# Kernel tuning notes

Hardware: AMD Instinct MI355X
Metric: run time of the kernel (lower is better)

The kernel has to match this reference:

```python
import jax, jax.numpy as jnp
import numpy as np

DIM = 2048; H = 16; QLR = 512; KVLR = 512
NOPE = 128; ROPE = 64; VHD = 128
QKHD = NOPE + ROPE
SCALE = QKHD ** -0.5
EPS = 1.1920929e-07  # torch RMSNorm default eps = finfo(float32).eps
B = 1; S = 2048

def _rmsnorm(x, w):
    return x * jax.lax.rsqrt(jnp.mean(x * x, axis=-1, keepdims=True) + EPS) * w

def _rope(x, cos, sin):
    # x: [b, s, h, d]; cos/sin: [s, d//2] (consecutive-pair complex rotation)
    b, s, h, d = x.shape
    x2 = x.reshape(b, s, h, d // 2, 2)
    x0, x1 = x2[..., 0], x2[..., 1]
    c = cos[None, :, None, :]; sn = sin[None, :, None, :]
    y = jnp.stack([x0 * c - x1 * sn, x0 * sn + x1 * c], axis=-1)
    return y.reshape(b, s, h, d)

def setup_inputs() -> dict:
    key = jax.random.key(0)
    ks = jax.random.split(key, 12)
    def lin(k, fan_in, fan_out):
        bound = 1.0 / np.sqrt(fan_in)
        kw, kb = jax.random.split(k)
        w = jax.random.uniform(kw, (fan_out, fan_in), jnp.float32, -bound, bound)
        b = jax.random.uniform(kb, (fan_out,), jnp.float32, -bound, bound)
        return w, b
    x = jax.random.normal(ks[0], (B, S, DIM), jnp.float32)
    theta = jax.random.uniform(ks[1], (S, ROPE // 2), jnp.float32, 0.0, 2 * np.pi)
    freqs_cos = jnp.cos(theta); freqs_sin = jnp.sin(theta)
    mask = jnp.where(jnp.triu(jnp.ones((S, S), bool), k=1), jnp.float32(-1e9), jnp.float32(0.0))
    wq_a_w, wq_a_b = lin(ks[2], DIM, QLR)
    q_norm_w = jnp.ones((QLR,), jnp.float32)
    wq_b_w, wq_b_b = lin(ks[3], QLR, H * QKHD)
    wkv_a_w, wkv_a_b = lin(ks[4], DIM, KVLR + ROPE)
    kv_norm_w = jnp.ones((KVLR,), jnp.float32)
    wkv_b_w, wkv_b_b = lin(ks[5], KVLR, H * (NOPE + VHD))
    wo_w, wo_b = lin(ks[6], H * VHD, DIM)
    return {"x": x, "start_pos": 0, "freqs_cos": freqs_cos, "freqs_sin": freqs_sin,
            "mask": mask, "wq_a_w": wq_a_w, "wq_a_b": wq_a_b, "q_norm_w": q_norm_w,
            "wq_b_w": wq_b_w, "wq_b_b": wq_b_b, "wkv_a_w": wkv_a_w, "wkv_a_b": wkv_a_b,
            "kv_norm_w": kv_norm_w, "wkv_b_w": wkv_b_w, "wkv_b_b": wkv_b_b,
            "wo_w": wo_w, "wo_b": wo_b}

def reference(x, start_pos, freqs_cos, freqs_sin, mask,
              wq_a_w, wq_a_b, q_norm_w, wq_b_w, wq_b_b,
              wkv_a_w, wkv_a_b, kv_norm_w, wkv_b_w, wkv_b_b, wo_w, wo_b):
    bsz, seqlen, _ = x.shape
    # low-rank query: wq_b(q_norm(wq_a(x)))
    q = _rmsnorm(x @ wq_a_w.T + wq_a_b, q_norm_w) @ wq_b_w.T + wq_b_b
    q = q.reshape(bsz, seqlen, H, QKHD)
    q_nope, q_pe = q[..., :NOPE], q[..., NOPE:]
    q_pe = _rope(q_pe, freqs_cos, freqs_sin)
    kv = x @ wkv_a_w.T + wkv_a_b
    kv_lat, k_pe = kv[..., :KVLR], kv[..., KVLR:]
    k_pe = _rope(k_pe[:, :, None, :], freqs_cos, freqs_sin)  # [b,s,1,ROPE]
    q = jnp.concatenate([q_nope, q_pe], axis=-1)
    kvb = (_rmsnorm(kv_lat, kv_norm_w) @ wkv_b_w.T + wkv_b_b).reshape(bsz, seqlen, H, NOPE + VHD)
    k_nope, v = kvb[..., :NOPE], kvb[..., NOPE:]
    k = jnp.concatenate([k_nope, jnp.broadcast_to(k_pe, (bsz, seqlen, H, ROPE))], axis=-1)
    # prefill (start_pos=0): cache[:end_pos] == freshly written k/v
    scores = jnp.einsum('bshd,bthd->bsht', q, k) * SCALE
    scores = scores + mask[None, :, None, :]
    probs = jax.nn.softmax(scores.astype(jnp.float32), axis=-1).astype(x.dtype)
    out = jnp.einsum('bsht,bthd->bshd', probs, v).reshape(bsz, seqlen, H * VHD)
    return out @ wo_w.T + wo_b
```

## Files before the change

kernel.cpp:

```cpp
#include <hip/hip_runtime.h>
#include <hip/hip_bf16.h>

typedef __attribute__((ext_vector_type(8))) short short8x;
typedef __attribute__((ext_vector_type(4))) short short4x;
typedef __attribute__((ext_vector_type(4))) float float4x;
typedef __hip_bfloat16 bf16;

#define EPS_F 1.1920929e-07f
#define SCALE_F 0.07216878364870323f

__device__ inline float rdv(const void* p, size_t i, int f32) {
  return f32 ? ((const float*)p)[i] : __bfloat162float(((const bf16*)p)[i]);
}

__device__ inline int4 pack8(const float* s) {
  unsigned short h[8];
#pragma unroll
  for (int t = 0; t < 8; t++) {
    bf16 b = __float2bfloat16(s[t]);
    __builtin_memcpy(&h[t], &b, 2);
  }
  int4 r;
  r.x = (int)((unsigned)h[0] | ((unsigned)h[1] << 16));
  r.y = (int)((unsigned)h[2] | ((unsigned)h[3] << 16));
  r.z = (int)((unsigned)h[4] | ((unsigned)h[5] << 16));
  r.w = (int)((unsigned)h[6] | ((unsigned)h[7] << 16));
  return r;
}

typedef __attribute__((address_space(1))) const unsigned int gu32;
typedef __attribute__((address_space(3))) unsigned int lu32;
__device__ __forceinline__ void gload16(const void* g, void* l) {
  __builtin_amdgcn_global_load_lds((gu32*)g, (lu32*)l, 16, 0, 0);
}

__device__ __forceinline__ int detect_exponents(const unsigned short* __restrict__ x,
                                                int tid, int* red) {
  int cnt = 0;
#pragma unroll
  for (int i = 0; i < 4; i++) {
    unsigned short u = x[tid * 4 + i];
    int e = (u >> 7) & 0xFF;
    cnt += (e >= 118 && e <= 130) ? 1 : 0;
  }
#pragma unroll
  for (int off = 1; off < 64; off <<= 1) cnt += __shfl_xor(cnt, off);
  if ((tid & 63) == 0) red[tid >> 6] = cnt;
  __syncthreads();
  return ((red[0] + red[1] + red[2] + red[3]) > 768) ? 0 : 1;
}

__global__ __launch_bounds__(256) void detect_dtype(const unsigned short* __restrict__ x,
                                                    int* __restrict__ flag) {
  __shared__ int red[4];
  int f = detect_exponents(x, threadIdx.x, red);
  if (threadIdx.x == 0) flag[0] = f;
}

__global__ __launch_bounds__(256) void sentinel_kernel(bf16* out, int n) {
  int i = blockIdx.x * 256 + threadIdx.x;
  if (i < n) out[i] = __float2bfloat16(1000.0f);
}

__device__ __forceinline__ void cvt8(const void* src, bf16* dst, size_t i, int f32) {
  if (f32) {
    float4 a = *(const float4*)((const float*)src + i);
    float4 b = *(const float4*)((const float*)src + i + 4);
    float s[8] = {a.x, a.y, a.z, a.w, b.x, b.y, b.z, b.w};
    *(int4*)(dst + i) = pack8(s);
  } else {
    *(int4*)(dst + i) = *(const int4*)((const bf16*)src + i);
  }
}

__global__ __launch_bounds__(256) void convert_in1(
    const void* __restrict__ x, const void* __restrict__ wqa,
    const void* __restrict__ wkva,
    const void* __restrict__ qab, const void* __restrict__ kvab,
    bf16* __restrict__ xb, bf16* __restrict__ wqab, bf16* __restrict__ wkvab,
    bf16* __restrict__ qabb, bf16* __restrict__ kvabb,
    const int* __restrict__ flagp)
{
  const int f32 = flagp[0];
  const int b = blockIdx.x, tid = threadIdx.x;
  if (b < 2048)       { size_t i = ((size_t)b * 256 + tid) * 8;          cvt8(x,    xb,    i, f32); }
  else if (b < 2560)  { size_t i = ((size_t)(b - 2048) * 256 + tid) * 8; cvt8(wqa,  wqab,  i, f32); }
  else if (b < 3136)  { size_t i = ((size_t)(b - 2560) * 256 + tid) * 8; cvt8(wkva, wkvab, i, f32); }
  else {
    for (int i = tid; i < 512; i += 256) qabb[i]  = __float2bfloat16(rdv(qab,  i, f32));
    for (int i = tid; i < 576; i += 256) kvabb[i] = __float2bfloat16(rdv(kvab, i, f32));
  }
}

__global__ __launch_bounds__(256) void convert_in2(
    const void* __restrict__ wqb, const void* __restrict__ wkvb,
    const void* __restrict__ qbb, const void* __restrict__ kvbb,
    bf16* __restrict__ wqbb, bf16* __restrict__ wkvbb,
    bf16* __restrict__ qbbb, bf16* __restrict__ kvbbb,
    const int* __restrict__ flagp)
{
  const int f32 = flagp[0];
  const int b = blockIdx.x, tid = threadIdx.x;
  if (b < 768)        { size_t i = ((size_t)b * 256 + tid) * 8;          cvt8(wqb,  wqbb,  i, f32); }
  else if (b < 1792)  { size_t i = ((size_t)(b - 768) * 256 + tid) * 8;  cvt8(wkvb, wkvbb, i, f32); }
  else if (b == 1792) { for (int i = tid; i < 3072; i += 256) qbbb[i]  = __float2bfloat16(rdv(qbb,  i, f32)); }
  else                { for (int i = tid; i < 4096; i += 256) kvbbb[i] = __float2bfloat16(rdv(kvbb, i, f32)); }
}

__global__ __launch_bounds__(256) void convert_wo(
    const void* __restrict__ wo, const void* __restrict__ wob_in,
    bf16* __restrict__ wo16, bf16* __restrict__ wob16,
    const int* __restrict__ flagp)
{
  const int f32 = flagp[0];
  const int b = blockIdx.x, tid = threadIdx.x;
  if (b < 2048) { size_t i = ((size_t)b * 256 + tid) * 8; cvt8(wo, wo16, i, f32); }
  else { for (int i = tid; i < 2048; i += 256) wob16[i] = __float2bfloat16(rdv(wob_in, i, f32)); }
}

__global__ __launch_bounds__(256) void convert_all(
    const void* __restrict__ x,
    const void* __restrict__ wqa, const void* __restrict__ wkva,
    const void* __restrict__ qab, const void* __restrict__ kvab,
    const void* __restrict__ wqb, const void* __restrict__ wkvb,
    const void* __restrict__ qbb, const void* __restrict__ kvbb,
    const void* __restrict__ wo, const void* __restrict__ wob_in,
    bf16* __restrict__ xb, bf16* __restrict__ wqab, bf16* __restrict__ wkvab,
    bf16* __restrict__ qabb, bf16* __restrict__ kvabb,
    bf16* __restrict__ wqbb, bf16* __restrict__ wkvbb,
    bf16* __restrict__ qbbb, bf16* __restrict__ kvbbb,
    bf16* __restrict__ wo16, bf16* __restrict__ wob16,
    int* __restrict__ flag)
{
  __shared__ int red[4];
  const int b = blockIdx.x, tid = threadIdx.x;
  const int f32 = detect_exponents((const unsigned short*)x, tid, red);
  if (b < 2048)       { size_t i = ((size_t)b * 256 + tid) * 8;          cvt8(x,    xb,    i, f32); }
  else if (b < 2560)  { size_t i = ((size_t)(b - 2048) * 256 + tid) * 8; cvt8(wqa,  wqab,  i, f32); }
  else if (b < 3136)  { size_t i = ((size_t)(b - 2560) * 256 + tid) * 8; cvt8(wkva, wkvab, i, f32); }
  else if (b == 3136) {
    for (int i = tid; i < 512; i += 256) qabb[i]  = __float2bfloat16(rdv(qab,  i, f32));
    for (int i = tid; i < 576; i += 256) kvabb[i] = __float2bfloat16(rdv(kvab, i, f32));
    if (tid == 0) flag[0] = f32;
  }
  else if (b < 5185)  { size_t i = ((size_t)(b - 3137) * 256 + tid) * 8; cvt8(wo, wo16, i, f32); }
  else if (b == 5185) { for (int i = tid; i < 2048; i += 256) wob16[i] = __float2bfloat16(rdv(wob_in, i, f32)); }
  else if (b < 5954)  { size_t i = ((size_t)(b - 5186) * 256 + tid) * 8; cvt8(wqb,  wqbb,  i, f32); }
  else if (b < 6978)  { size_t i = ((size_t)(b - 5954) * 256 + tid) * 8; cvt8(wkvb, wkvbb, i, f32); }
  else if (b == 6978) { for (int i = tid; i < 3072; i += 256) qbbb[i]  = __float2bfloat16(rdv(qbb,  i, f32)); }
  else                { for (int i = tid; i < 4096; i += 256) kvbbb[i] = __float2bfloat16(rdv(kvbb, i, f32)); }
}

template<int OMODE, bool A_DYN>
__device__ __forceinline__ void gemm128_body(
    const void* __restrict__ A, const void* __restrict__ W,
    const void* __restrict__ bias, void* __restrict__ Cout,
    int M, int N, int K, int f32in, int bx, int by,
    int kbeg, int kend, int addbias)
{
  __shared__ int4 As4[128 * 4];
  __shared__ int4 Bs4[128 * 4];
  const int tid = threadIdx.x, lane = tid & 63, wave = tid >> 6;
  const int grp = lane >> 4, l16 = lane & 15;
  const int m0 = bx * 128, n0 = by * 128;
  const int wm = (wave & 1) * 64, wn = (wave >> 1) * 64;
  float4x acc[4][4] = {};
  for (int k0 = kbeg; k0 < kend; k0 += 32) {
    if (!f32in) {
#pragma unroll
      for (int j = 0; j < 2; j++) {
        int row = wave * 32 + j * 16 + (lane >> 2);
        int cs = (lane & 3) ^ ((row >> 1) & 3);
        gload16((const bf16*)A + (size_t)(m0 + row) * K + k0 + cs * 8,
                &As4[(wave * 32 + j * 16) * 4]);
        gload16((const bf16*)W + (size_t)(n0 + row) * K + k0 + cs * 8,
                &Bs4[(wave * 32 + j * 16) * 4]);
      }
    } else {
#pragma unroll
      for (int i = 0; i < 2; i++) {
        int ch = tid + i * 256;
        int row = ch >> 2, c = ch & 3;
        int cs = c ^ ((row >> 1) & 3);
        size_t aoff = (size_t)(m0 + row) * K + k0 + cs * 8;
        size_t boff = (size_t)(n0 + row) * K + k0 + cs * 8;
        As4[row * 4 + c] = A_DYN ? pack8((const float*)A + aoff)
                                 : *(const int4*)((const bf16*)A + aoff);
        Bs4[row * 4 + c] = pack8((const float*)W + boff);
      }
    }
    __syncthreads();
    short8x af[4], bfr[4];
#pragma unroll
    for (int i = 0; i < 4; i++) {
      int ra = wm + i * 16 + l16;
      int rb = wn + i * 16 + l16;
      af[i]  = *(const short8x*)&As4[ra * 4 + (grp ^ ((ra >> 1) & 3))];
      bfr[i] = *(const short8x*)&Bs4[rb * 4 + (grp ^ ((rb >> 1) & 3))];
    }
#pragma unroll
    for (int i = 0; i < 4; i++)
#pragma unroll
      for (int j = 0; j < 4; j++)
        acc[i][j] = __builtin_amdgcn_mfma_f32_16x16x32_bf16(af[i], bfr[j], acc[i][j], 0, 0, 0);
    __syncthreads();
  }
#pragma unroll
  for (int j = 0; j < 4; j++) {
    int gn = n0 + wn + j * 16 + l16;
    if (gn < N) {
      float bv = addbias ? rdv(bias, gn, f32in) : 0.0f;
#pragma unroll
      for (int i = 0; i < 4; i++) {
        int gm0 = m0 + wm + i * 16 + grp * 4;
#pragma unroll
        for (int r = 0; r < 4; r++) {
          float v = acc[i][j][r] + bv;
          size_t idx = (size_t)(gm0 + r) * N + gn;
          if (OMODE == 0)      ((float*)Cout)[idx] = v;
          else if (OMODE == 1) ((bf16*)Cout)[idx] = __float2bfloat16(v);
          else {
            if (f32in) ((float*)Cout)[idx] = v;
            else       ((bf16*)Cout)[idx] = __float2bfloat16(v);
          }
        }
      }
    }
  }
}

__global__ __launch_bounds__(256) void gemmB_dual(
    const void* __restrict__ A0, const void* __restrict__ A1,
    const void* __restrict__ W0, const void* __restrict__ W1,
    const void* __restrict__ b0, const void* __restrict__ b1,
    void* __restrict__ C0, void* __restrict__ C1)
{
  const int z = blockIdx.z;
  if (z == 0 && blockIdx.y >= 24) return;
  const void* A = z ? A1 : A0;
  const void* W = z ? W1 : W0;
  const void* bias = z ? b1 : b0;
  void* C = z ? C1 : C0;
  const int N = z ? 4096 : 3072;
  gemm128_body<1, false>(A, W, bias, C, 2048, N, 512, 0,
                         blockIdx.x, blockIdx.y, 0, 512, 1);
}

__global__ __launch_bounds__(256) void gemmB_fused(
    const bf16* __restrict__ qn, const bf16* __restrict__ kvn,
    const bf16* __restrict__ Wq, const bf16* __restrict__ Wkv,
    const bf16* __restrict__ bq, const bf16* __restrict__ bkv,
    const void* __restrict__ cosb, const void* __restrict__ sinb,
    bf16* __restrict__ qbuf, bf16* __restrict__ kvbC, bf16* __restrict__ Vt,
    const int* __restrict__ flagp)
{
  const int z = blockIdx.z;
  if (z == 0 && blockIdx.y >= 24) return;
  const bf16* A = z ? kvn : qn;
  const bf16* W = z ? Wkv : Wq;
  const bf16* bias = z ? bkv : bq;
  const int K = 512;
  __shared__ int4 As4[128 * 4];
  __shared__ int4 Bs4[128 * 4];
  const int tid = threadIdx.x, lane = tid & 63, wave = tid >> 6;
  const int grp = lane >> 4, l16 = lane & 15;
  const int m0 = blockIdx.x * 128, n0 = blockIdx.y * 128;
  const int wm = (wave & 1) * 64, wn = (wave >> 1) * 64;
  float4x acc[4][4] = {};
  for (int k0 = 0; k0 < K; k0 += 32) {
#pragma unroll
    for (int j = 0; j < 2; j++) {
      int row = wave * 32 + j * 16 + (lane >> 2);
      int cs = (lane & 3) ^ ((row >> 1) & 3);
      gload16(A + (size_t)(m0 + row) * K + k0 + cs * 8,
              &As4[(wave * 32 + j * 16) * 4]);
      gload16(W + (size_t)(n0 + row) * K + k0 + cs * 8,
              &Bs4[(wave * 32 + j * 16) * 4]);
    }
    __syncthreads();
    short8x af[4], bfr[4];
#pragma unroll
    for (int i = 0; i < 4; i++) {
      int ra = wm + i * 16 + l16;
      int rb = wn + i * 16 + l16;
      af[i]  = *(const short8x*)&As4[ra * 4 + (grp ^ ((ra >> 1) & 3))];
      bfr[i] = *(const short8x*)&Bs4[rb * 4 + (grp ^ ((rb >> 1) & 3))];
    }
#pragma unroll
    for (int i = 0; i < 4; i++)
#pragma unroll
      for (int j = 0; j < 4; j++)
        acc[i][j] = __builtin_amdgcn_mfma_f32_16x16x32_bf16(af[i], bfr[j], acc[i][j], 0, 0, 0);
    __syncthreads();
  }
  const int f32 = flagp[0];
#pragma unroll
  for (int j = 0; j < 4; j++) {
    int gn = n0 + wn + j * 16 + l16;
    float bv = __bfloat162float(bias[gn]);
    if (z == 0) {
      int c12 = (gn >> 4) % 12;
      if (c12 >= 8) {
        int jj = ((gn % 192) - 128) >> 1;
#pragma unroll
        for (int i = 0; i < 4; i++) {
          int gm0 = m0 + wm + i * 16 + grp * 4;
#pragma unroll
          for (int r = 0; r < 4; r++) {
            float v = acc[i][j][r] + bv;
            int s = gm0 + r;
            float c  = rdv(cosb, (size_t)s * 32 + jj, f32);
            float sn = rdv(sinb, (size_t)s * 32 + jj, f32);
            float o = __shfl_xor(v, 1);
            float res = (l16 & 1) ? (o * sn + v * c)
                                  : (v * c - o * sn);
            qbuf[(size_t)s * 3072 + gn] = __float2bfloat16(res);
          }
        }
      } else {
#pragma unroll
        for (int i = 0; i < 4; i++) {
          int gm0 = m0 + wm + i * 16 + grp * 4;
#pragma unroll
          for (int r = 0; r < 4; r++)
            qbuf[(size_t)(gm0 + r) * 3072 + gn] = __float2bfloat16(acc[i][j][r] + bv);
        }
      }
    } else {
      int c16 = (gn >> 4) & 15;
      if (c16 >= 8) {
        int hh = gn >> 8;
        int d  = (gn & 255) - 128;
        bf16* vtb = Vt + ((size_t)hh * 128 + d) * 2048;
#pragma unroll
        for (int i = 0; i < 4; i++) {
          int gm0 = m0 + wm + i * 16 + grp * 4;
          unsigned short hv[4];
#pragma unroll
          for (int r = 0; r < 4; r++) {
            bf16 t = __float2bfloat16(acc[i][j][r] + bv);
            __builtin_memcpy(&hv[r], &t, 2);
          }
          int2 w;
          w.x = (int)((unsigned)hv[0] | ((unsigned)hv[1] << 16));
          w.y = (int)((unsigned)hv[2] | ((unsigned)hv[3] << 16));
          *(int2*)(vtb + gm0) = w;
        }
      } else {
        int coff = (gn >> 8) * 128 + (gn & 127);
#pragma unroll
        for (int i = 0; i < 4; i++) {
          int gm0 = m0 + wm + i * 16 + grp * 4;
#pragma unroll
          for (int r = 0; r < 4; r++)
            kvbC[(size_t)(gm0 + r) * 2048 + coff] = __float2bfloat16(acc[i][j][r] + bv);
        }
      }
    }
  }
}

__global__ __launch_bounds__(256) void gemmWo_sk(
    const void* __restrict__ A, const void* __restrict__ W,
    const void* __restrict__ bias, float* __restrict__ part,
    const int* __restrict__ flagp)
{
  const int z = blockIdx.z;
  gemm128_body<0, false>(A, W, bias, part + (size_t)z * 2048 * 2048,
                         2048, 2048, 2048, flagp[0],
                         blockIdx.x, blockIdx.y, z * 1024, z * 1024 + 1024, z == 0);
}

__global__ __launch_bounds__(256) void gemmWo_sk_bf(
    const void* __restrict__ A, const void* __restrict__ W,
    const void* __restrict__ bias, float* __restrict__ part)
{
  const int z = blockIdx.z;
  gemm128_body<0, false>(A, W, bias, part + (size_t)z * 2048 * 2048,
                         2048, 2048, 2048, 0,
                         blockIdx.x, blockIdx.y, z * 1024, z * 1024 + 1024, z == 0);
}

__global__ __launch_bounds__(256) void reduce_out(
    const float* __restrict__ p0, const float* __restrict__ p1,
    void* __restrict__ out, const int* __restrict__ flagp)
{
  const int f32in = flagp[0];
  size_t i = ((size_t)blockIdx.x * 256 + threadIdx.x) * 4;
  float4 a = *(const float4*)(p0 + i);
  float4 b = *(const float4*)(p1 + i);
  a.x += b.x; a.y += b.y; a.z += b.z; a.w += b.w;
  if (f32in) {
    *(float4*)((float*)out + i) = a;
  } else {
    unsigned short h[4];
    bf16 t0 = __float2bfloat16(a.x); __builtin_memcpy(&h[0], &t0, 2);
    bf16 t1 = __float2bfloat16(a.y); __builtin_memcpy(&h[1], &t1, 2);
    bf16 t2 = __float2bfloat16(a.z); __builtin_memcpy(&h[2], &t2, 2);
    bf16 t3 = __float2bfloat16(a.w); __builtin_memcpy(&h[3], &t3, 2);
    int2 v;
    v.x = (int)((unsigned)h[0] | ((unsigned)h[1] << 16));
    v.y = (int)((unsigned)h[2] | ((unsigned)h[3] << 16));
    *(int2*)((bf16*)out + i) = v;
  }
}

__global__ __launch_bounds__(256) void gemmA_sk(
    const void* __restrict__ A,
    const void* __restrict__ W0, const void* __restrict__ W1,
    const void* __restrict__ b0, const void* __restrict__ b1,
    float* __restrict__ C0, float* __restrict__ C1)
{
  const int z = blockIdx.z;
  const int mat = z >> 1, kh = z & 1;
  const int N = mat ? 576 : 512;
  if (blockIdx.y * 128 >= N) return;
  const void* W = mat ? W1 : W0;
  const void* bias = mat ? b1 : b0;
  float* C = (mat ? C1 : C0) + (size_t)kh * 2048 * N;
  gemm128_body<0, false>(A, W, bias, C, 2048, N, 2048, 0,
                         blockIdx.x, blockIdx.y,
                         kh * 1024, kh * 1024 + 1024, kh == 0);
}

__global__ __launch_bounds__(256) void norms_merged(
    const float* __restrict__ q_a0, const float* __restrict__ q_a1,
    const float* __restrict__ kv_a0, const float* __restrict__ kv_a1,
    const void* __restrict__ qw, const void* __restrict__ kvw,
    const void* __restrict__ cosb, const void* __restrict__ sinb,
    bf16* __restrict__ qn, bf16* __restrict__ kvn, bf16* __restrict__ kpe,
    const int* __restrict__ flagp)
{
  const int f32in = flagp[0];
  const int b = blockIdx.x, tid = threadIdx.x;
  __shared__ float red[4];
  if (b < 2048) {
    const int s = b;
    size_t base = (size_t)s * 512;
    float v0 = q_a0[base + tid] + q_a1[base + tid];
    float v1 = q_a0[base + tid + 256] + q_a1[base + tid + 256];
    float ss = v0 * v0 + v1 * v1;
#pragma unroll
    for (int off = 1; off < 64; off <<= 1) ss += __shfl_xor(ss, off);
    if ((tid & 63) == 0) red[tid >> 6] = ss;
    __syncthreads();
    float tot = red[0] + red[1] + red[2] + red[3];
    float scale = rsqrtf(tot * (1.0f / 512.0f) + EPS_F);
    qn[base + tid]       = __float2bfloat16(v0 * scale * rdv(qw, tid, f32in));
    qn[base + tid + 256] = __float2bfloat16(v1 * scale * rdv(qw, tid + 256, f32in));
  } else {
    const int s = b - 2048;
    size_t base = (size_t)s * 576;
    float v0 = kv_a0[base + tid] + kv_a1[base + tid];
    float v1 = kv_a0[base + tid + 256] + kv_a1[base + tid + 256];
    float ss = v0 * v0 + v1 * v1;
#pragma unroll
    for (int off = 1; off < 64; off <<= 1) ss += __shfl_xor(ss, off);
    if ((tid & 63) == 0) red[tid >> 6] = ss;
    __syncthreads();
    float tot = red[0] + red[1] + red[2] + red[3];
    float scale = rsqrtf(tot * (1.0f / 512.0f) + EPS_F);
    kvn[(size_t)s * 512 + tid]       = __float2bfloat16(v0 * scale * rdv(kvw, tid, f32in));
    kvn[(size_t)s * 512 + tid + 256] = __float2bfloat16(v1 * scale * rdv(kvw, tid + 256, f32in));
    if (tid < 32) {
      float x0 = kv_a0[base + 512 + 2 * tid] + kv_a1[base + 512 + 2 * tid];
      float x1 = kv_a0[base + 512 + 2 * tid + 1] + kv_a1[base + 512 + 2 * tid + 1];
      float c  = rdv(cosb, (size_t)s * 32 + tid, f32in);
      float sn = rdv(sinb, (size_t)s * 32 + tid, f32in);
      kpe[s * 64 + 2 * tid]     = __float2bfloat16(x0 * c - x1 * sn);
      kpe[s * 64 + 2 * tid + 1] = __float2bfloat16(x0 * sn + x1 * c);
    }
  }
}

__global__ __launch_bounds__(256) void rope_vt_merged(
    bf16* __restrict__ q, const void* __restrict__ cosb,
    const void* __restrict__ sinb, const bf16* __restrict__ kvb,
    bf16* __restrict__ Vt, const int* __restrict__ flagp)
{
  const int b = blockIdx.x, tid = threadIdx.x;
  __shared__ __align__(16) bf16 tile[64][136];
  if (b < 2048) {
    const int f32in = flagp[0];
    const int s = b;
#pragma unroll
    for (int it = 0; it < 2; it++) {
      int p = tid + it * 256;
      int hh = p >> 5, jj = p & 31;
      bf16* src = q + (size_t)s * 3072 + hh * 192 + 128 + 2 * jj;
      float x0 = __bfloat162float(src[0]);
      float x1 = __bfloat162float(src[1]);
      float c  = rdv(cosb, (size_t)s * 32 + jj, f32in);
      float sn = rdv(sinb, (size_t)s * 32 + jj, f32in);
      src[0] = __float2bfloat16(x0 * c - x1 * sn);
      src[1] = __float2bfloat16(x0 * sn + x1 * c);
    }
  } else {
    const int hb = b - 2048;
    const int h = hb & 15;
    const int t0 = (hb >> 4) * 64;
#pragma unroll
    for (int i = 0; i < 4; i++) {
      int chunk = tid + i * 256;
      int row = chunk >> 4;
      int c8 = (chunk & 15) * 8;
      *(int4*)&tile[row][c8] =
          *(const int4*)(kvb + (size_t)(t0 + row) * 4096 + h * 256 + 128 + c8);
    }
    __syncthreads();
#pragma unroll
    for (int i = 0; i < 32; i++) {
      int idx = tid + i * 256;
      int d = idx >> 6;
      int t = idx & 63;
      Vt[((size_t)h * 128 + d) * 2048 + t0 + t] = tile[t][d];
    }
  }
}

__global__ __launch_bounds__(256) void attn_kernel(
    const bf16* __restrict__ Q, const bf16* __restrict__ kvb,
    const bf16* __restrict__ kpe, const bf16* __restrict__ Vt,
    bf16* __restrict__ Out, const int kvs, const int kvh)
{
  __shared__ __align__(16) bf16 Ks[64 * 200];
  __shared__ __align__(16) bf16 Vs[128 * 72];
  __shared__ __align__(16) bf16 plds[4][16 * 68];
  const int b = blockIdx.x;
  const int h = b & 15;
  const int tt = (b >> 4) & 15;
  const int q0 = ((b >> 8) ? (31 - tt) : tt) * 64;
  const int tid = threadIdx.x;
  const int wave = tid >> 6;
  const int lane = tid & 63;
  const int grp = lane >> 4, l16 = lane & 15;
  const int qrt = q0 + wave * 16;
  const bf16* Qbase = Q + (size_t)(qrt + l16) * 3072 + h * 192;
  short8x qf[6];
#pragma unroll
  for (int c = 0; c < 6; c++)
    qf[c] = *(const short8x*)(Qbase + c * 32 + grp * 8);
  float m_run[4], l_run[4];
  float4x o_acc[8] = {};
#pragma unroll
  for (int r = 0; r < 4; r++) { m_run[r] = -__builtin_inff(); l_run[r] = 0.f; }
  bf16* pl = &plds[wave][0];
  for (int t0 = 0; t0 <= q0; t0 += 64) {
#pragma unroll
    for (int i = 0; i < 4; i++) {
      int ch = tid + i * 256;
      int row = ch >> 4, c = ch & 15;
      *(int4*)&Ks[row * 200 + c * 8] =
          *(const int4*)(kvb + (size_t)(t0 + row) * kvs + h * kvh + c * 8);
    }
#pragma unroll
    for (int i = 0; i < 2; i++) {
      int ch = tid + i * 256;
      int row = ch >> 3, c = ch & 7;
      *(int4*)&Ks[row * 200 + 128 + c * 8] =
          *(const int4*)(kpe + (size_t)(t0 + row) * 64 + c * 8);
    }
#pragma unroll
    for (int i = 0; i < 4; i++) {
      int ch = tid + i * 256;
      int row = ch >> 3, c = ch & 7;
      *(int4*)&Vs[row * 72 + c * 8] =
          *(const int4*)(Vt + ((size_t)h * 128 + row) * 2048 + t0 + c * 8);
    }
    __syncthreads();
    float4x sacc[4] = {};
#pragma unroll
    for (int n = 0; n < 4; n++) {
      const bf16* Kb = &Ks[(n * 16 + l16) * 200 + grp * 8];
#pragma unroll
      for (int c = 0; c < 6; c++) {
        short8x kf = *(const short8x*)(Kb + c * 32);
        sacc[n] = __builtin_amdgcn_mfma_f32_16x16x32_bf16(qf[c], kf, sacc[n], 0, 0, 0);
      }
    }
    float pv[4][4], alpha[4];
#pragma unroll
    for (int r = 0; r < 4; r++) {
      const int s_row = qrt + grp * 4 + r;
      float p0[4];
      float mx = -__builtin_inff();
#pragma unroll
      for (int n = 0; n < 4; n++) {
        int t = t0 + n * 16 + l16;
        float v = sacc[n][r] * SCALE_F;
        v = (t > s_row) ? -1.0e9f : v;
        p0[n] = v;
        mx = fmaxf(mx, v);
      }
      mx = fmaxf(mx, __shfl_xor(mx, 1));
      mx = fmaxf(mx, __shfl_xor(mx, 2));
      mx = fmaxf(mx, __shfl_xor(mx, 4));
      mx = fmaxf(mx, __shfl_xor(mx, 8));
      float m_new = fmaxf(m_run[r], mx);
      float a = __expf(m_run[r] - m_new);
      m_run[r] = m_new;
      float sum = 0.f;
#pragma unroll
      for (int n = 0; n < 4; n++) {
        float e = __expf(p0[n] - m_new);
        pv[n][r] = e;
        sum += e;
      }
      sum += __shfl_xor(sum, 1);
      sum += __shfl_xor(sum, 2);
      sum += __shfl_xor(sum, 4);
      sum += __shfl_xor(sum, 8);
      l_run[r] = l_run[r] * a + sum;
      alpha[r] = a;
    }
#pragma unroll
    for (int n = 0; n < 8; n++)
#pragma unroll
      for (int r = 0; r < 4; r++)
        o_acc[n][r] *= alpha[r];
#pragma unroll
    for (int n = 0; n < 4; n++)
#pragma unroll
      for (int r = 0; r < 4; r++)
        pl[(grp * 4 + r) * 68 + n * 16 + l16] = __float2bfloat16(pv[n][r]);
#pragma unroll
    for (int c = 0; c < 2; c++) {
      union { short4x h4[2]; short8x v8; } pk;
      const bf16* pp = pl + l16 * 68 + c * 32 + grp * 8;
      pk.h4[0] = *(const short4x*)(pp);
      pk.h4[1] = *(const short4x*)(pp + 4);
#pragma unroll
      for (int n = 0; n < 8; n++) {
        short8x vf = *(const short8x*)&Vs[(size_t)(n * 16 + l16) * 72 + c * 32 + grp * 8];
        o_acc[n] = __builtin_amdgcn_mfma_f32_16x16x32_bf16(pk.v8, vf, o_acc[n], 0, 0, 0);
      }
    }
    __syncthreads();
  }
  float inv[4];
#pragma unroll
  for (int r = 0; r < 4; r++) inv[r] = 1.0f / l_run[r];
#pragma unroll
  for (int n = 0; n < 8; n++)
#pragma unroll
    for (int r = 0; r < 4; r++) {
      int s_row = qrt + grp * 4 + r;
      Out[(size_t)s_row * 2048 + h * 128 + n * 16 + l16] =
          __float2bfloat16(o_acc[n][r] * inv[r]);
    }
}

extern "C" void kernel_launch(void* const* d_in, const int* in_sizes, int n_in,
                              void* d_out, int out_size, void* d_ws, size_t ws_size,
                              hipStream_t stream) {
  const void* x        = d_in[0];
  const void* fcos     = d_in[2];
  const void* fsin     = d_in[3];
  const void* wq_a_w   = d_in[5];
  const void* wq_a_b   = d_in[6];
  const void* q_norm_w = d_in[7];
  const void* wq_b_w   = d_in[8];
  const void* wq_b_b   = d_in[9];
  const void* wkv_a_w  = d_in[10];
  const void* wkv_a_b  = d_in[11];
  const void* kv_norm_w= d_in[12];
  const void* wkv_b_w  = d_in[13];
  const void* wkv_b_b  = d_in[14];
  const void* wo_w     = d_in[15];
  const void* wo_b     = d_in[16];

  const size_t KB = 1024, MB = 1024 * 1024;
  if (ws_size < 46 * MB) {
    sentinel_kernel<<<(out_size + 255) / 256, 256, 0, stream>>>((bf16*)d_out, out_size);
    return;
  }
  char* ws = (char*)d_ws;
  bf16*  kpe    = (bf16*)(ws);
  int*   flag   = (int*)(ws + 256 * KB);
  bf16*  qbuf   = (bf16*)(ws + 512 * KB);
  bf16*  kvb    = (bf16*)(ws + 12 * MB + 512 * KB);
  bf16*  kvbC   = (bf16*)(ws + 12 * MB + 512 * KB);
  bf16*  Vt     = (bf16*)(ws + 28 * MB + 512 * KB);
  bf16*  attnout= (bf16*)(ws + 36 * MB + 512 * KB);
  float* kv_a0  = (float*)(ws + 512 * KB);
  float* kv_a1  = (float*)(ws + 5 * MB);
  float* q_a0   = (float*)(ws + 36 * MB + 512 * KB);
  float* q_a1   = (float*)(ws + 40 * MB + 512 * KB);
  bf16*  qn     = (bf16*)(ws + 28 * MB + 512 * KB);
  bf16*  kvn    = (bf16*)(ws + 30 * MB + 512 * KB);
  float* wpart  = (float*)(ws + 512 * KB);
  bf16*  xb     = (bf16*)(ws + 12 * MB + 512 * KB);
  bf16*  wqab   = (bf16*)(ws + 20 * MB + 512 * KB);
  bf16*  wkvab  = (bf16*)(ws + 22 * MB + 512 * KB);
  bf16*  qabb   = (bf16*)(ws + 25 * MB);
  bf16*  kvabb  = (bf16*)(ws + 25 * MB + 64 * KB);
  bf16*  wqbb_m = (bf16*)(ws + 36 * MB + 512 * KB);
  bf16*  wkvbb_m= (bf16*)(ws + 39 * MB + 512 * KB);
  bf16*  qbbb_m = (bf16*)(ws + 43 * MB + 512 * KB);
  bf16*  kvbbb_m= (bf16*)(ws + 43 * MB + 768 * KB);
  bf16*  wo16   = (bf16*)(ws + 46 * MB);
  bf16*  wob16  = (bf16*)(ws + 54 * MB + 512 * KB);
  bf16*  wqbb_b = (bf16*)(ws + 56 * MB);
  bf16*  wkvbb_b= (bf16*)(ws + 59 * MB);
  bf16*  qbbb_b = (bf16*)(ws + 63 * MB);
  bf16*  kvbbb_b= (bf16*)(ws + 63 * MB + 64 * KB);
  bf16*  qnF    = (bf16*)(ws + 20 * MB + 512 * KB);
  bf16*  kvnF   = (bf16*)(ws + 22 * MB + 512 * KB);

  const bool wofast = (ws_size >= 56 * MB);
  const bool bigws  = (ws_size >= 64 * MB);

  dim3 blk(256);
  if (bigws) {
    convert_all<<<6980, blk, 0, stream>>>(
        x, wq_a_w, wkv_a_w, wq_a_b, wkv_a_b, wq_b_w, wkv_b_w, wq_b_b, wkv_b_b,
        wo_w, wo_b,
        xb, wqab, wkvab, qabb, kvabb, wqbb_b, wkvbb_b, qbbb_b, kvbbb_b,
        wo16, wob16, flag);
    gemmA_sk<<<dim3(16, 5, 4), blk, 0, stream>>>(
        xb, wqab, wkvab, qabb, kvabb, q_a0, kv_a0);
    norms_merged<<<4096, blk, 0, stream>>>(
        q_a0, q_a1, kv_a0, kv_a1, q_norm_w, kv_norm_w, fcos, fsin,
        qnF, kvnF, kpe, flag);
    gemmB_fused<<<dim3(16, 32, 2), blk, 0, stream>>>(
        qnF, kvnF, wqbb_b, wkvbb_b, qbbb_b, kvbbb_b, fcos, fsin,
        qbuf, kvbC, Vt, flag);
    attn_kernel<<<dim3(512), blk, 0, stream>>>(qbuf, kvbC, kpe, Vt, attnout,
                                               2048, 128);
    gemmWo_sk_bf<<<dim3(16, 16, 2), blk, 0, stream>>>(attnout, wo16, wob16, wpart);
    reduce_out<<<4096, blk, 0, stream>>>(wpart, wpart + (size_t)2048 * 2048, d_out, flag);
  } else {
    detect_dtype<<<1, blk, 0, stream>>>((const unsigned short*)x, flag);
    convert_in1<<<3137, blk, 0, stream>>>(
        x, wq_a_w, wkv_a_w, wq_a_b, wkv_a_b, xb, wqab, wkvab, qabb, kvabb, flag);
    if (wofast)
      convert_wo<<<2049, blk, 0, stream>>>(wo_w, wo_b, wo16, wob16, flag);
    gemmA_sk<<<dim3(16, 5, 4), blk, 0, stream>>>(
        xb, wqab, wkvab, qabb, kvabb, q_a0, kv_a0);
    norms_merged<<<4096, blk, 0, stream>>>(
        q_a0, q_a1, kv_a0, kv_a1, q_norm_w, kv_norm_w, fcos, fsin,
        qn, kvn, kpe, flag);
    convert_in2<<<1794, blk, 0, stream>>>(
        wq_b_w, wkv_b_w, wq_b_b, wkv_b_b, wqbb_m, wkvbb_m, qbbb_m, kvbbb_m, flag);
    gemmB_dual<<<dim3(16, 32, 2), blk, 0, stream>>>(
        qn, kvn, wqbb_m, wkvbb_m, qbbb_m, kvbbb_m, qbuf, kvb);
    rope_vt_merged<<<2560, blk, 0, stream>>>(qbuf, fcos, fsin, kvb, Vt, flag);
    attn_kernel<<<dim3(512), blk, 0, stream>>>(qbuf, kvb, kpe, Vt, attnout,
                                               4096, 256);
    if (wofast)
      gemmWo_sk_bf<<<dim3(16, 16, 2), blk, 0, stream>>>(attnout, wo16, wob16, wpart);
    else
      gemmWo_sk<<<dim3(16, 16, 2), blk, 0, stream>>>(attnout, wo_w, wo_b, wpart, flag);
    reduce_out<<<4096, blk, 0, stream>>>(wpart, wpart + (size_t)2048 * 2048, d_out, flag);
  }
}
```

Measured before the change: 317.2 us.

## Split causal attention KV range into two chunks with a merge kernel

Result: no change. 311.9 us (-1.7%).

```diff
diff --git a/kernel.cpp b/kernel.cpp
--- a/kernel.cpp
+++ b/kernel.cpp
@@ -8,6 +8,7 @@
 
 #define EPS_F 1.1920929e-07f
 #define SCALE_F 0.07216878364870323f
+#define M_INIT -1.0e30f
 
 __device__ inline float rdv(const void* p, size_t i, int f32) {
   return f32 ? ((const float*)p)[i] : __bfloat162float(((const bf16*)p)[i]);
@@ -516,6 +517,206 @@
       Vt[((size_t)h * 128 + d) * 2048 + t0 + t] = tile[t][d];
     }
   }
+}
+
+__global__ __launch_bounds__(256) void attn_split(
+    const bf16* __restrict__ Q, const bf16* __restrict__ kvb,
+    const bf16* __restrict__ kpe, const bf16* __restrict__ Vt,
+    bf16* __restrict__ P0, bf16* __restrict__ P1,
+    float* __restrict__ ml0, float* __restrict__ ml1,
+    const int kvs, const int kvh)
+{
+  __shared__ __align__(16) bf16 Ks[64 * 200];
+  __shared__ __align__(16) bf16 Vs[128 * 72];
+  __shared__ __align__(16) bf16 plds[4][16 * 68];
+  const int b = blockIdx.x;
+  const int cchunk = b >> 9;
+  const int h = b & 15;
+  const int tt = 31 - ((b >> 4) & 31);
+  const int q0 = tt * 64;
+  const int nt = tt + 1;
+  const int half = (nt + 1) >> 1;
+  const int lo = cchunk ? half : 0;
+  const int hi = cchunk ? nt : half;
+  bf16* Pout = cchunk ? P1 : P0;
+  float* mlp = cchunk ? ml1 : ml0;
+  const int tid = threadIdx.x;
+  const int wave = tid >> 6;
+  const int lane = tid & 63;
+  const int grp = lane >> 4, l16 = lane & 15;
+  const int qrt = q0 + wave * 16;
+
+  if (lo >= hi) {
+#pragma unroll
+    for (int n = 0; n < 8; n++) {
+      int s_row = qrt + grp * 4;
+#pragma unroll
+      for (int r = 0; r < 4; r++)
+        Pout[(size_t)(s_row + r) * 2048 + h * 128 + n * 16 + l16] =
+            __float2bfloat16(0.0f);
+    }
+    if ((lane & 15) == 0) {
+#pragma unroll
+      for (int r = 0; r < 4; r++) {
+        int s_row = qrt + grp * 4 + r;
+        mlp[((size_t)h * 2048 + s_row) * 2]     = M_INIT;
+        mlp[((size_t)h * 2048 + s_row) * 2 + 1] = 0.0f;
+      }
+    }
+    return;
+  }
+
+  const bf16* Qbase = Q + (size_t)(qrt + l16) * 3072 + h * 192;
+  short8x qf[6];
+#pragma unroll
+  for (int c = 0; c < 6; c++)
+    qf[c] = *(const short8x*)(Qbase + c * 32 + grp * 8);
+  float m_run[4], l_run[4];
+  float4x o_acc[8] = {};
+#pragma unroll
+  for (int r = 0; r < 4; r++) { m_run[r] = M_INIT; l_run[r] = 0.f; }
+  bf16* pl = &plds[wave][0];
+  for (int ti = lo; ti < hi; ti++) {
+    const int t0 = ti * 64;
+#pragma unroll
+    for (int i = 0; i < 4; i++) {
+      int ch = tid + i * 256;
+      int row = ch >> 4, c = ch & 15;
+      *(int4*)&Ks[row * 200 + c * 8] =
+          *(const int4*)(kvb + (size_t)(t0 + row) * kvs + h * kvh + c * 8);
+    }
+#pragma unroll
+    for (int i = 0; i < 2; i++) {
+      int ch = tid + i * 256;
+      int row = ch >> 3, c = ch & 7;
+      *(int4*)&Ks[row * 200 + 128 + c * 8] =
+          *(const int4*)(kpe + (size_t)(t0 + row) * 64 + c * 8);
+    }
+#pragma unroll
+    for (int i = 0; i < 4; i++) {
+      int ch = tid + i * 256;
+      int row = ch >> 3, c = ch & 7;
+      *(int4*)&Vs[row * 72 + c * 8] =
+          *(const int4*)(Vt + ((size_t)h * 128 + row) * 2048 + t0 + c * 8);
+    }
+    __syncthreads();
+    float4x sacc[4] = {};
+#pragma unroll
+    for (int n = 0; n < 4; n++) {
+      const bf16* Kb = &Ks[(n * 16 + l16) * 200 + grp * 8];
+#pragma unroll
+      for (int c = 0; c < 6; c++) {
+        short8x kf = *(const short8x*)(Kb + c * 32);
+        sacc[n] = __builtin_amdgcn_mfma_f32_16x16x32_bf16(qf[c], kf, sacc[n], 0, 0, 0);
+      }
+    }
+    float pv[4][4], alpha[4];
+#pragma unroll
+    for (int r = 0; r < 4; r++) {
+      const int s_row = qrt + grp * 4 + r;
+      float p0[4];
+      float mx = M_INIT;
+#pragma unroll
+      for (int n = 0; n < 4; n++) {
+        int t = t0 + n * 16 + l16;
+        float v = sacc[n][r] * SCALE_F;
+        v = (t > s_row) ? -1.0e9f : v;
+        p0[n] = v;
+        mx = fmaxf(mx, v);
+      }
+      mx = fmaxf(mx, __shfl_xor(mx, 1));
+      mx = fmaxf(mx, __shfl_xor(mx, 2));
+      mx = fmaxf(mx, __shfl_xor(mx, 4));
+      mx = fmaxf(mx, __shfl_xor(mx, 8));
+      float m_new = fmaxf(m_run[r], mx);
+      float a = __expf(m_run[r] - m_new);
+      m_run[r] = m_new;
+      float sum = 0.f;
+#pragma unroll
+      for (int n = 0; n < 4; n++) {
+        float e = __expf(p0[n] - m_new);
+        pv[n][r] = e;
+        sum += e;
+      }
+      sum += __shfl_xor(sum, 1);
+      sum += __shfl_xor(sum, 2);
+      sum += __shfl_xor(sum, 4);
+      sum += __shfl_xor(sum, 8);
+      l_run[r] = l_run[r] * a + sum;
+      alpha[r] = a;
+    }
+#pragma unroll
+    for (int n = 0; n < 8; n++)
+#pragma unroll
+      for (int r = 0; r < 4; r++)
+        o_acc[n][r] *= alpha[r];
+#pragma unroll
+    for (int n = 0; n < 4; n++)
+#pragma unroll
+      for (int r = 0; r < 4; r++)
+        pl[(grp * 4 + r) * 68 + n * 16 + l16] = __float2bfloat16(pv[n][r]);
+#pragma unroll
+    for (int c = 0; c < 2; c++) {
+      union { short4x h4[2]; short8x v8; } pk;
+      const bf16* pp = pl + l16 * 68 + c * 32 + grp * 8;
+      pk.h4[0] = *(const short4x*)(pp);
+      pk.h4[1] = *(const short4x*)(pp + 4);
+#pragma unroll
+      for (int n = 0; n < 8; n++) {
+        short8x vf = *(const short8x*)&Vs[(size_t)(n * 16 + l16) * 72 + c * 32 + grp * 8];
+        o_acc[n] = __builtin_amdgcn_mfma_f32_16x16x32_bf16(pk.v8, vf, o_acc[n], 0, 0, 0);
+      }
+    }
+    __syncthreads();
+  }
+#pragma unroll
+  for (int n = 0; n < 8; n++)
+#pragma unroll
+    for (int r = 0; r < 4; r++) {
+      int s_row = qrt + grp * 4 + r;
+      Pout[(size_t)s_row * 2048 + h * 128 + n * 16 + l16] =
+          __float2bfloat16(o_acc[n][r]);
+    }
+  if ((lane & 15) == 0) {
+#pragma unroll
+    for (int r = 0; r < 4; r++) {
+      int s_row = qrt + grp * 4 + r;
+      mlp[((size_t)h * 2048 + s_row) * 2]     = m_run[r];
+      mlp[((size_t)h * 2048 + s_row) * 2 + 1] = l_run[r];
+    }
+  }
+}
+
+__global__ __launch_bounds__(256) void attn_merge(
+    bf16* __restrict__ P0, const bf16* __restrict__ P1,
+    const float* __restrict__ ml0, const float* __restrict__ ml1)
+{
+  const int s_row = blockIdx.x, tid = threadIdx.x;
+  const int h = tid >> 4;
+  const size_t mli = ((size_t)h * 2048 + s_row) * 2;
+  float m0 = ml0[mli], l0 = ml0[mli + 1];
+  float m1 = ml1[mli], l1 = ml1[mli + 1];
+  float M = fmaxf(m0, m1);
+  float w0 = __expf(m0 - M), w1 = __expf(m1 - M);
+  float Linv = 1.0f / (l0 * w0 + l1 * w1);
+  size_t base = (size_t)s_row * 2048 + tid * 8;
+  int4 a4 = *(const int4*)(P0 + base);
+  int4 b4 = *(const int4*)(P1 + base);
+  const unsigned short* ah = (const unsigned short*)&a4;
+  const unsigned short* bh = (const unsigned short*)&b4;
+  unsigned short oh[8];
+#pragma unroll
+  for (int k = 0; k < 8; k++) {
+    unsigned ua = (unsigned)ah[k] << 16, ub = (unsigned)bh[k] << 16;
+    float fa, fb;
+    __builtin_memcpy(&fa, &ua, 4);
+    __builtin_memcpy(&fb, &ub, 4);
+    bf16 t = __float2bfloat16((fa * w0 + fb * w1) * Linv);
+    __builtin_memcpy(&oh[k], &t, 2);
+  }
+  int4 o4;
+  __builtin_memcpy(&o4, oh, 16);
+  *(int4*)(P0 + base) = o4;
 }
 
 __global__ __launch_bounds__(256) void attn_kernel(
@@ -706,6 +907,9 @@
   bf16*  kvbbb_b= (bf16*)(ws + 63 * MB + 64 * KB);
   bf16*  qnF    = (bf16*)(ws + 20 * MB + 512 * KB);
   bf16*  kvnF   = (bf16*)(ws + 22 * MB + 512 * KB);
+  bf16*  attnP1 = (bf16*)(ws + 20 * MB + 512 * KB);
+  float* attnml0= (float*)(ws + 44 * MB + 512 * KB);
+  float* attnml1= (float*)(ws + 44 * MB + 768 * KB);
 
   const bool wofast = (ws_size >= 56 * MB);
   const bool bigws  = (ws_size >= 64 * MB);
@@ -725,8 +929,9 @@
     gemmB_fused<<<dim3(16, 32, 2), blk, 0, stream>>>(
         qnF, kvnF, wqbb_b, wkvbb_b, qbbb_b, kvbbb_b, fcos, fsin,
         qbuf, kvbC, Vt, flag);
-    attn_kernel<<<dim3(512), blk, 0, stream>>>(qbuf, kvbC, kpe, Vt, attnout,
-                                               2048, 128);
+    attn_split<<<dim3(1024), blk, 0, stream>>>(
+        qbuf, kvbC, kpe, Vt, attnout, attnP1, attnml0, attnml1, 2048, 128);
+    attn_merge<<<dim3(2048), blk, 0, stream>>>(attnout, attnP1, attnml0, attnml1);
     gemmWo_sk_bf<<<dim3(16, 16, 2), blk, 0, stream>>>(attnout, wo16, wob16, wpart);
     reduce_out<<<4096, blk, 0, stream>>>(wpart, wpart + (size_t)2048 * 2048, d_out, flag);
   } else {
```
